# Kernel tuning notes

Measured on AMD Instinct MI355X. Metric: run time of the kernel, lower is better.

Reference implementation:

```python
import jax, jax.numpy as jnp
import numpy as np

N = 20000      # nodes
E = 320000     # edges (before self-loops)
F_IN = 512     # input feature size
HID = 128      # encoder hidden
OUT = 128      # encoder output / GAT in_channels
H = 4          # gat heads
C = 64         # gat out_channels per head


def setup_inputs() -> dict:
    key = jax.random.key(0)
    ks = jax.random.split(key, 10)
    s = 0.05
    return {
        "x": jax.random.normal(ks[0], (N, F_IN), jnp.float32),
        "edge_index": jax.random.randint(ks[1], (2, E), 0, N, dtype=jnp.int64),
        "W1": jax.random.normal(ks[2], (F_IN, HID), jnp.float32) * s,
        "b1": jax.random.normal(ks[3], (HID,), jnp.float32) * s,
        "W2": jax.random.normal(ks[4], (HID, OUT), jnp.float32) * s,
        "b2": jax.random.normal(ks[5], (OUT,), jnp.float32) * s,
        "Wg": jax.random.normal(ks[6], (OUT, H * C), jnp.float32) * s,
        "att_src": jax.random.normal(ks[7], (H, C), jnp.float32) * s,
        "att_dst": jax.random.normal(ks[8], (H, C), jnp.float32) * s,
        "bias_g": jax.random.normal(ks[9], (H * C,), jnp.float32) * s,
    }


def reference(x, edge_index, W1, b1, W2, b2, Wg, att_src, att_dst, bias_g):
    # MLP encoder: Linear -> ReLU -> Linear
    h = jnp.maximum(x @ W1 + b1, 0.0) @ W2 + b2            # [N, OUT]

    # GATConv (concat=True, eval mode -> no dropout)
    xg = (h @ Wg).reshape(N, H, C)                          # per-head projections

    # add self-loops (PyG GATConv default)
    loops = jnp.arange(N, dtype=edge_index.dtype)
    src = jnp.concatenate([edge_index[0], loops])           # [E+N] source j
    dst = jnp.concatenate([edge_index[1], loops])           # [E+N] dest   i

    a_src = jnp.einsum('nhc,hc->nh', xg, att_src)           # [N, H]
    a_dst = jnp.einsum('nhc,hc->nh', xg, att_dst)           # [N, H]

    e = jax.nn.leaky_relu(a_src[src] + a_dst[dst], 0.2)     # [E+N, H]

    # segment softmax over incoming edges of each destination node
    m = jax.ops.segment_max(e, dst, num_segments=N)         # [N, H]
    ex = jnp.exp(e - m[dst])
    denom = jax.ops.segment_sum(ex, dst, num_segments=N)
    alpha = ex / (denom[dst] + 1e-16)                       # [E+N, H]

    # weighted scatter-add aggregation
    out = jax.ops.segment_sum(alpha[:, :, None] * xg[src], dst, num_segments=N)  # [N, H, C]
    return out.reshape(N, H * C) + bias_g
```

## Files before the change

kernel.cpp:

```cpp
#include <hip/hip_runtime.h>
#include <math.h>

#define NNODES 20000
#define NEDGES 320000
#define FIN    512
#define HIDD   128
#define OUTD   128
#define NH     4
#define NC     64
#define HC     256

typedef short bf16x8 __attribute__((ext_vector_type(8)));
typedef float f32x4  __attribute__((ext_vector_type(4)));

__device__ __forceinline__ unsigned short f2bf(float f) {
    unsigned int u = __float_as_uint(f);
    unsigned int r = 0x7fffu + ((u >> 16) & 1u);
    return (unsigned short)((u + r) >> 16);
}
__device__ __forceinline__ float b2f(short t) {
    return __uint_as_float(((unsigned)(unsigned short)t) << 16);
}
__device__ __forceinline__ float4 f4max(float4 a, float4 b) {
    return make_float4(fmaxf(a.x,b.x), fmaxf(a.y,b.y), fmaxf(a.z,b.z), fmaxf(a.w,b.w));
}
__device__ __forceinline__ float4 f4add(float4 a, float4 b) {
    return make_float4(a.x+b.x, a.y+b.y, a.z+b.z, a.w+b.w);
}
__device__ __forceinline__ float4 f4sub(float4 a, float4 b) {
    return make_float4(a.x-b.x, a.y-b.y, a.z-b.z, a.w-b.w);
}
__device__ __forceinline__ float4 f4mul(float4 a, float4 b) {
    return make_float4(a.x*b.x, a.y*b.y, a.z*b.z, a.w*b.w);
}
__device__ __forceinline__ float4 f4exp(float4 a) {
    return make_float4(__expf(a.x), __expf(a.y), __expf(a.z), __expf(a.w));
}
__device__ __forceinline__ float4 shflx4(float4 v, int m) {
    return make_float4(__shfl_xor(v.x,m), __shfl_xor(v.y,m), __shfl_xor(v.z,m), __shfl_xor(v.w,m));
}

__global__ __launch_bounds__(256)
void prep_kernel(const float* __restrict__ W1, unsigned short* __restrict__ W1t,
                 const float* __restrict__ W2, const float* __restrict__ b2,
                 const float* __restrict__ Wg, unsigned short* __restrict__ W2gt,
                 float* __restrict__ b2g, int* __restrict__ deg, int n) {
    const int T1 = FIN * HIDD;
    const int T2 = HC * HIDD;
    int idx = blockIdx.x * 256 + threadIdx.x;
    if (idx < T1) {
        int nn = idx / FIN, k = idx % FIN;
        W1t[idx] = f2bf(W1[(size_t)k * HIDD + nn]);
    } else if (idx < T1 + T2) {
        int local = idx - T1;
        int nn = local >> 7;
        int k  = local & 127;
        float s = 0.f;
        #pragma unroll 8
        for (int t = 0; t < HIDD; ++t)
            s += W2[(size_t)k * OUTD + t] * Wg[(size_t)t * HC + nn];
        W2gt[(size_t)nn * HIDD + k] = f2bf(s);
        if (k == 0) {
            float t2 = 0.f;
            #pragma unroll 8
            for (int t = 0; t < OUTD; ++t) t2 += b2[t] * Wg[(size_t)t * HC + nn];
            b2g[nn] = t2;
        }
    } else if (idx < T1 + T2 + n) {
        deg[idx - T1 - T2] = 1;
    }
}

__global__ __launch_bounds__(256)
void gemm1_count_kernel(const float* __restrict__ A,
                        const unsigned short* __restrict__ Bt,
                        const float* __restrict__ bias,
                        unsigned short* __restrict__ C,
                        const int* __restrict__ dst, int* __restrict__ deg,
                        int M, int E, int gemmBlocks) {
    __shared__ unsigned short As[32 * 64];
    __shared__ unsigned short Bs[128 * 64];

    if ((int)blockIdx.x >= gemmBlocks) {
        int i = ((int)blockIdx.x - gemmBlocks) * 256 + threadIdx.x;
        if (i < E) atomicAdd(&deg[dst[i]], 1);
        return;
    }

    const int tid  = threadIdx.x;
    const int lane = tid & 63;
    const int w    = tid >> 6;
    const int wr   = w >> 1;
    const int wc   = w & 1;
    const int m0   = blockIdx.x * 32;

    char* pA = (char*)As;
    char* pB = (char*)Bs;

    f32x4 acc[4];
    #pragma unroll
    for (int n = 0; n < 4; ++n) acc[n] = (f32x4){0.f, 0.f, 0.f, 0.f};

    for (int k0 = 0; k0 < FIN; k0 += 64) {
        {
            const int row = tid >> 3;
            const int sg  = tid & 7;
            const bool ok = (m0 + row) < M;
            const float4* Ap = (const float4*)(A + (size_t)(m0 + row) * FIN + k0 + sg * 8);
            float4 f0 = make_float4(0,0,0,0), f1 = f0;
            if (ok) { f0 = Ap[0]; f1 = Ap[1]; }
            unsigned short u[8];
            u[0]=f2bf(f0.x); u[1]=f2bf(f0.y); u[2]=f2bf(f0.z); u[3]=f2bf(f0.w);
            u[4]=f2bf(f1.x); u[5]=f2bf(f1.y); u[6]=f2bf(f1.z); u[7]=f2bf(f1.w);
            *(bf16x8*)(pA + (((row * 128 + sg * 16)) ^ ((row & 7) << 4))) = *(bf16x8*)&u[0];
        }
        #pragma unroll
        for (int i = 0; i < 4; ++i) {
            int s   = tid + i * 256;
            int col = s >> 3;
            int sg  = s & 7;
            bf16x8 v = *(const bf16x8*)(Bt + (size_t)col * FIN + k0 + sg * 8);
            *(bf16x8*)(pB + (((col * 128 + sg * 16)) ^ ((col & 7) << 4))) = v;
        }
        __syncthreads();

        #pragma unroll
        for (int ks = 0; ks < 2; ++ks) {
            const int kb = ks * 64 + ((lane >> 4) << 4);
            int row = wr * 16 + (lane & 15);
            bf16x8 a = *(const bf16x8*)(pA + ((row * 128 + kb) ^ ((row & 7) << 4)));
            bf16x8 b[4];
            #pragma unroll
            for (int n = 0; n < 4; ++n) {
                int col = wc * 64 + n * 16 + (lane & 15);
                b[n] = *(const bf16x8*)(pB + ((col * 128 + kb) ^ ((col & 7) << 4)));
            }
            #pragma unroll
            for (int n = 0; n < 4; ++n)
                acc[n] = __builtin_amdgcn_mfma_f32_16x16x32_bf16(a, b[n], acc[n], 0, 0, 0);
        }
        __syncthreads();
    }

    #pragma unroll
    for (int n = 0; n < 4; ++n) {
        const int col = wc * 64 + n * 16 + (lane & 15);
        const float bv = bias[col];
        #pragma unroll
        for (int r = 0; r < 4; ++r) {
            const int row = m0 + wr * 16 + ((lane >> 4) << 2) + r;
            if (row >= M) continue;
            float v = fmaxf(acc[n][r] + bv, 0.f);
            C[(size_t)row * HIDD + col] = f2bf(v);
        }
    }
}

__global__ __launch_bounds__(256)
void gemm2_dots_kernel(const unsigned short* __restrict__ Ab,
                       const unsigned short* __restrict__ Bt,
                       const float* __restrict__ b2g,
                       const float* __restrict__ att_src,
                       const float* __restrict__ att_dst,
                       unsigned short* __restrict__ xgb,
                       float* __restrict__ a_src, float* __restrict__ a_dst,
                       int M) {
    __shared__ unsigned short As[64 * 64];
    __shared__ unsigned short Bs[128 * 64];

    const int tid  = threadIdx.x;
    const int lane = tid & 63;
    const int w    = tid >> 6;
    const int wr   = w >> 1;
    const int wc   = w & 1;
    const int m0   = blockIdx.x * 64;
    const int n0   = blockIdx.y * 128;

    char* pA = (char*)As;
    char* pB = (char*)Bs;

    f32x4 acc[2][4];
    #pragma unroll
    for (int m = 0; m < 2; ++m)
        #pragma unroll
        for (int n = 0; n < 4; ++n) acc[m][n] = (f32x4){0.f, 0.f, 0.f, 0.f};

    for (int k0 = 0; k0 < HIDD; k0 += 64) {
        #pragma unroll
        for (int i = 0; i < 2; ++i) {
            int s   = tid + i * 256;
            int row = s >> 3;
            int sg  = s & 7;
            bf16x8 v = {};
            if ((m0 + row) < M)
                v = *(const bf16x8*)(Ab + (size_t)(m0 + row) * HIDD + k0 + sg * 8);
            *(bf16x8*)(pA + (((row * 128 + sg * 16)) ^ ((row & 7) << 4))) = v;
        }
        #pragma unroll
        for (int i = 0; i < 4; ++i) {
            int s   = tid + i * 256;
            int col = s >> 3;
            int sg  = s & 7;
            bf16x8 v = *(const bf16x8*)(Bt + (size_t)(n0 + col) * HIDD + k0 + sg * 8);
            *(bf16x8*)(pB + (((col * 128 + sg * 16)) ^ ((col & 7) << 4))) = v;
        }
        __syncthreads();

        #pragma unroll
        for (int ks = 0; ks < 2; ++ks) {
            const int kb = ks * 64 + ((lane >> 4) << 4);
            bf16x8 a[2], b[4];
            #pragma unroll
            for (int m = 0; m < 2; ++m) {
                int row = wr * 32 + m * 16 + (lane & 15);
                a[m] = *(const bf16x8*)(pA + ((row * 128 + kb) ^ ((row & 7) << 4)));
            }
            #pragma unroll
            for (int n = 0; n < 4; ++n) {
                int col = wc * 64 + n * 16 + (lane & 15);
                b[n] = *(const bf16x8*)(pB + ((col * 128 + kb) ^ ((col & 7) << 4)));
            }
            #pragma unroll
            for (int m = 0; m < 2; ++m)
                #pragma unroll
                for (int n = 0; n < 4; ++n)
                    acc[m][n] = __builtin_amdgcn_mfma_f32_16x16x32_bf16(
                        a[m], b[n], acc[m][n], 0, 0, 0);
        }
        __syncthreads();
    }

    const int head = blockIdx.y * 2 + wc;
    const int cIn  = lane & 15;
    float ds_p[2][4], dd_p[2][4];
    #pragma unroll
    for (int m = 0; m < 2; ++m)
        #pragma unroll
        for (int r = 0; r < 4; ++r) { ds_p[m][r] = 0.f; dd_p[m][r] = 0.f; }

    #pragma unroll
    for (int n = 0; n < 4; ++n) {
        const int ch  = n * 16 + cIn;
        const int col = n0 + wc * 64 + n * 16 + cIn;
        const float bv   = b2g[col];
        const float as_c = att_src[head * NC + ch];
        const float ad_c = att_dst[head * NC + ch];
        #pragma unroll
        for (int m = 0; m < 2; ++m) {
            #pragma unroll
            for (int r = 0; r < 4; ++r) {
                const int row = m0 + wr * 32 + m * 16 + ((lane >> 4) << 2) + r;
                float v = acc[m][n][r] + bv;
                if (row < M) xgb[(size_t)row * HC + col] = f2bf(v);
                ds_p[m][r] += v * as_c;
                dd_p[m][r] += v * ad_c;
            }
        }
    }
    #pragma unroll
    for (int m = 0; m < 2; ++m) {
        #pragma unroll
        for (int r = 0; r < 4; ++r) {
            float s = ds_p[m][r], d = dd_p[m][r];
            s += __shfl_xor(s, 1); s += __shfl_xor(s, 2);
            s += __shfl_xor(s, 4); s += __shfl_xor(s, 8);
            d += __shfl_xor(d, 1); d += __shfl_xor(d, 2);
            d += __shfl_xor(d, 4); d += __shfl_xor(d, 8);
            if (cIn == 0) {
                const int row = m0 + wr * 32 + m * 16 + ((lane >> 4) << 2) + r;
                if (row < M) {
                    a_src[row * NH + head] = s;
                    a_dst[row * NH + head] = d;
                }
            }
        }
    }
}

__global__ __launch_bounds__(1024)
void scan_offsets_kernel(const int* __restrict__ deg, int* __restrict__ offs,
                         int* __restrict__ cursor, int n) {
    __shared__ int wsum[16], wbase[16];
    const int tid = threadIdx.x, lane = tid & 63, w = tid >> 6;
    const int i0 = tid * 20;
    int loc[20];
    int s = 0;
    #pragma unroll
    for (int k = 0; k < 20; ++k) {
        int i = i0 + k;
        int v = (i < n) ? deg[i] : 0;
        loc[k] = s;
        s += v;
    }
    int incl = s;
    #pragma unroll
    for (int d = 1; d < 64; d <<= 1) {
        int t = __shfl_up(incl, d);
        if (lane >= d) incl += t;
    }
    if (lane == 63) wsum[w] = incl;
    __syncthreads();
    if (w == 0) {
        int v = (lane < 16) ? wsum[lane] : 0;
        int sc = v;
        #pragma unroll
        for (int d = 1; d < 16; d <<= 1) {
            int t = __shfl_up(sc, d);
            if (lane >= d) sc += t;
        }
        if (lane < 16) wbase[lane] = sc - v;
    }
    __syncthreads();
    const int excl = wbase[w] + incl - s;
    #pragma unroll
    for (int k = 0; k < 20; ++k) {
        int i = i0 + k;
        if (i < n) { int o = excl + loc[k]; offs[i] = o; cursor[i] = o; }
    }
    if (tid == 1023) offs[n] = excl + s;
}

__global__ void scatter_kernel(const int* __restrict__ src, const int* __restrict__ dst,
                               int* __restrict__ cursor, int* __restrict__ csr_src,
                               int e, int n) {
    int i = blockIdx.x * 256 + threadIdx.x;
    if (i < e) {
        int s = src[i], d = dst[i];
        csr_src[atomicAdd(&cursor[d], 1)] = s;
    } else if (i < e + n) {
        int node = i - e;
        csr_src[atomicAdd(&cursor[node], 1)] = node;
    }
}

__global__ __launch_bounds__(256)
void gat_aggregate4_kernel(const unsigned short* __restrict__ xgb,
                           const float4* __restrict__ asrc4,
                           const float4* __restrict__ adst4,
                           const int* __restrict__ offs, const int* __restrict__ csr_src,
                           const float* __restrict__ bias, float* __restrict__ out, int n) {
    __shared__ float4 exbuf[4][64];
    __shared__ int    sbuf[4][64];
    const int wv   = threadIdx.x >> 6;
    const int lane = threadIdx.x & 63;
    const int node = blockIdx.x * 4 + wv;
    if (node >= n) return;
    const int beg = offs[node], end = offs[node + 1];
    const int deg = end - beg;
    const float4 adstv = adst4[node];

    float4 m   = make_float4(-INFINITY, -INFINITY, -INFINITY, -INFINITY);
    float4 den = make_float4(0.f, 0.f, 0.f, 0.f);
    for (int c0 = 0; c0 < deg; c0 += 64) {
        int idx = beg + c0 + lane;
        bool ok = idx < end;
        int s = ok ? csr_src[idx] : 0;
        float4 e = make_float4(-INFINITY, -INFINITY, -INFINITY, -INFINITY);
        if (ok) {
            float4 a = asrc4[s];
            e = f4add(a, adstv);
            e.x = e.x > 0.f ? e.x : 0.2f * e.x;
            e.y = e.y > 0.f ? e.y : 0.2f * e.y;
            e.z = e.z > 0.f ? e.z : 0.2f * e.z;
            e.w = e.w > 0.f ? e.w : 0.2f * e.w;
        }
        float4 cm = e;
        #pragma unroll
        for (int dd = 32; dd >= 1; dd >>= 1) cm = f4max(cm, shflx4(cm, dd));
        float4 nm = f4max(m, cm);
        float4 ex = f4exp(f4sub(e, nm));
        exbuf[wv][lane] = ex;
        sbuf[wv][lane]  = s;
        float4 cs = ex;
        #pragma unroll
        for (int dd = 32; dd >= 1; dd >>= 1) cs = f4add(cs, shflx4(cs, dd));
        den = f4add(f4mul(den, f4exp(f4sub(m, nm))), cs);
        m = nm;
    }

    const int hi = lane >> 5;
    const int ll = lane & 31;
    const int h  = ll >> 3;
    const float denh = (h == 0) ? den.x : (h == 1) ? den.y : (h == 2) ? den.z : den.w;
    const float inv = 1.f / (denh + 1e-16f);

    float4 acc0 = make_float4(0.f, 0.f, 0.f, 0.f);
    float4 acc1 = make_float4(0.f, 0.f, 0.f, 0.f);
    const float* exf = (const float*)&exbuf[wv][0];

    auto do_edge = [&](int jj) {
        int s = sbuf[wv][jj];
        float wgt = exf[jj * 4 + h];
        bf16x8 v = *(const bf16x8*)(xgb + (size_t)s * HC + ll * 8);
        acc0.x += wgt * b2f(v[0]); acc0.y += wgt * b2f(v[1]);
        acc0.z += wgt * b2f(v[2]); acc0.w += wgt * b2f(v[3]);
        acc1.x += wgt * b2f(v[4]); acc1.y += wgt * b2f(v[5]);
        acc1.z += wgt * b2f(v[6]); acc1.w += wgt * b2f(v[7]);
    };

    auto run_chunk = [&](int cn) {
        int j = 0;
        for (; j + 16 <= cn; j += 16) {
            int ss[8]; float ww[8]; bf16x8 vv[8];
            #pragma unroll
            for (int t = 0; t < 8; ++t) {
                int jj = j + 2 * t + hi;
                ss[t] = sbuf[wv][jj];
                ww[t] = exf[jj * 4 + h];
            }
            #pragma unroll
            for (int t = 0; t < 8; ++t)
                vv[t] = *(const bf16x8*)(xgb + (size_t)ss[t] * HC + ll * 8);
            #pragma unroll
            for (int t = 0; t < 8; ++t) {
                acc0.x += ww[t]*b2f(vv[t][0]); acc0.y += ww[t]*b2f(vv[t][1]);
                acc0.z += ww[t]*b2f(vv[t][2]); acc0.w += ww[t]*b2f(vv[t][3]);
                acc1.x += ww[t]*b2f(vv[t][4]); acc1.y += ww[t]*b2f(vv[t][5]);
                acc1.z += ww[t]*b2f(vv[t][6]); acc1.w += ww[t]*b2f(vv[t][7]);
            }
        }
        for (; j + 8 <= cn; j += 8) {
            do_edge(j + hi);     do_edge(j + 2 + hi);
            do_edge(j + 4 + hi); do_edge(j + 6 + hi);
        }
        for (; j + 4 <= cn; j += 4) {
            do_edge(j + hi);
            do_edge(j + 2 + hi);
        }
        for (; j < cn; j += 2) {
            int jj = j + hi;
            if (jj < cn) do_edge(jj);
        }
    };

    if (deg <= 64) {
        run_chunk(deg);
    } else {
        for (int c0 = 0; c0 < deg; c0 += 64) {
            int idx = beg + c0 + lane;
            if (idx < end) {
                int s = csr_src[idx];
                float4 e = f4add(asrc4[s], adstv);
                e.x = e.x > 0.f ? e.x : 0.2f * e.x;
                e.y = e.y > 0.f ? e.y : 0.2f * e.y;
                e.z = e.z > 0.f ? e.z : 0.2f * e.z;
                e.w = e.w > 0.f ? e.w : 0.2f * e.w;
                exbuf[wv][lane] = f4exp(f4sub(e, m));
                sbuf[wv][lane]  = s;
            }
            int cn = deg - c0; if (cn > 64) cn = 64;
            run_chunk(cn);
        }
    }

    acc0.x += __shfl_xor(acc0.x, 32); acc0.y += __shfl_xor(acc0.y, 32);
    acc0.z += __shfl_xor(acc0.z, 32); acc0.w += __shfl_xor(acc0.w, 32);
    acc1.x += __shfl_xor(acc1.x, 32); acc1.y += __shfl_xor(acc1.y, 32);
    acc1.z += __shfl_xor(acc1.z, 32); acc1.w += __shfl_xor(acc1.w, 32);

    const float4* b4 = (const float4*)bias;
    float4* op = (float4*)(out + (size_t)node * HC);
    if (hi == 0) {
        float4 bv = b4[ll * 2];
        op[ll * 2] = make_float4(acc0.x * inv + bv.x, acc0.y * inv + bv.y,
                                 acc0.z * inv + bv.z, acc0.w * inv + bv.w);
    } else {
        float4 bv = b4[ll * 2 + 1];
        op[ll * 2 + 1] = make_float4(acc1.x * inv + bv.x, acc1.y * inv + bv.y,
                                     acc1.z * inv + bv.z, acc1.w * inv + bv.w);
    }
}

extern "C" void kernel_launch(void* const* d_in, const int* in_sizes, int n_in,
                              void* d_out, int out_size, void* d_ws, size_t ws_size,
                              hipStream_t stream) {
    const float* x       = (const float*)d_in[0];
    const int*   ei      = (const int*)d_in[1];
    const float* W1      = (const float*)d_in[2];
    const float* b1      = (const float*)d_in[3];
    const float* W2      = (const float*)d_in[4];
    const float* b2      = (const float*)d_in[5];
    const float* Wg      = (const float*)d_in[6];
    const float* att_src = (const float*)d_in[7];
    const float* att_dst = (const float*)d_in[8];
    const float* bias_g  = (const float*)d_in[9];

    const int Nn = in_sizes[0] / FIN;
    const int E  = in_sizes[1] / 2;
    const int* e_src = ei;
    const int* e_dst = ei + E;

    char* w = (char*)d_ws;
    auto alloc = [&](size_t bytes) { char* p = w; w += (bytes + 255) & ~(size_t)255; return p; };
    unsigned short* W1t  = (unsigned short*)alloc((size_t)OUTD * FIN * 2);
    unsigned short* W2gt = (unsigned short*)alloc((size_t)HC * HIDD * 2);
    float* b2g  = (float*)alloc(HC * 4);
    unsigned short* h1  = (unsigned short*)alloc((size_t)Nn * HIDD * 2);
    unsigned short* xgb = (unsigned short*)alloc((size_t)Nn * HC * 2);
    float* asrc = (float*)alloc((size_t)Nn * NH * 4);
    float* adst = (float*)alloc((size_t)Nn * NH * 4);
    int* deg    = (int*)alloc((size_t)Nn * 4);
    int* offs   = (int*)alloc((size_t)(Nn + 1) * 4);
    int* cursor = (int*)alloc((size_t)Nn * 4);
    int* csr    = (int*)alloc((size_t)(E + Nn) * 4);

    dim3 blk(256);

    {
        int total = FIN * HIDD + HC * HIDD + Nn;
        prep_kernel<<<dim3((total + 255) / 256), blk, 0, stream>>>(
            W1, W1t, W2, b2, Wg, W2gt, b2g, deg, Nn);
    }

    {
        int gb = (Nn + 31) / 32;
        int cb = (E + 255) / 256;
        gemm1_count_kernel<<<dim3(gb + cb), blk, 0, stream>>>(
            x, W1t, b1, h1, e_dst, deg, Nn, E, gb);
    }

    gemm2_dots_kernel<<<dim3((Nn + 63) / 64, 2), blk, 0, stream>>>(
        h1, W2gt, b2g, att_src, att_dst, xgb, asrc, adst, Nn);

    scan_offsets_kernel<<<dim3(1), dim3(1024), 0, stream>>>(deg, offs, cursor, Nn);
    scatter_kernel<<<dim3((E + Nn + 255) / 256), blk, 0, stream>>>(
        e_src, e_dst, cursor, csr, E, Nn);

    gat_aggregate4_kernel<<<dim3((Nn + 3) / 4), blk, 0, stream>>>(
        xgb, (const float4*)asrc, (const float4*)adst, offs, csr, bias_g,
        (float*)d_out, Nn);
}
```

Baseline: 127.0 us.

## Fold degree scan into gemm2 launch, pre-place self-loops, tile W1 transpose

The single-block prefix scan of node degrees now runs as an extra block inside the gemm2 launch instead of as its own kernel. That block writes each node's self-loop entry directly into the CSR and starts the cursor one past it, so the scatter kernel only handles real edges. The W1 transpose in the prep kernel now goes through a 32x32 shared-memory tile so both reads and writes are coalesced. This removes one launch and some atomics. The cost is that the scan becomes a serial loop over 256-element chunks in one block, which could become the slowest block of the gemm2 grid.

```diff
diff --git a/kernel.cpp b/kernel.cpp
--- a/kernel.cpp
+++ b/kernel.cpp
@@ -40,19 +40,35 @@
     return make_float4(__shfl_xor(v.x,m), __shfl_xor(v.y,m), __shfl_xor(v.z,m), __shfl_xor(v.w,m));
 }
 
+#define PREP_TB1 64
+#define PREP_TB2 192
 __global__ __launch_bounds__(256)
 void prep_kernel(const float* __restrict__ W1, unsigned short* __restrict__ W1t,
                  const float* __restrict__ W2, const float* __restrict__ b2,
                  const float* __restrict__ Wg, unsigned short* __restrict__ W2gt,
                  float* __restrict__ b2g, int* __restrict__ deg, int n) {
-    const int T1 = FIN * HIDD;
-    const int T2 = HC * HIDD;
-    int idx = blockIdx.x * 256 + threadIdx.x;
-    if (idx < T1) {
-        int nn = idx / FIN, k = idx % FIN;
-        W1t[idx] = f2bf(W1[(size_t)k * HIDD + nn]);
-    } else if (idx < T1 + T2) {
-        int local = idx - T1;
+    const int bid = blockIdx.x;
+    const int tid = threadIdx.x;
+    if (bid < PREP_TB1) {
+        __shared__ float tile[32][33];
+        const int tk = bid >> 2;
+        const int tn = bid & 3;
+        const int k0 = tk * 32, n0 = tn * 32;
+        const int nin = tid & 31;
+        const int r8  = tid >> 5;
+        #pragma unroll
+        for (int s = 0; s < 4; ++s) {
+            int k = s * 8 + r8;
+            tile[k][nin] = W1[(size_t)(k0 + k) * HIDD + n0 + nin];
+        }
+        __syncthreads();
+        #pragma unroll
+        for (int s = 0; s < 4; ++s) {
+            int nn = s * 8 + r8;
+            W1t[(size_t)(n0 + nn) * FIN + k0 + nin] = f2bf(tile[nin][nn]);
+        }
+    } else if (bid < PREP_TB2) {
+        int local = (bid - PREP_TB1) * 256 + tid;
         int nn = local >> 7;
         int k  = local & 127;
         float s = 0.f;
@@ -66,8 +82,9 @@
             for (int t = 0; t < OUTD; ++t) t2 += b2[t] * Wg[(size_t)t * HC + nn];
             b2g[nn] = t2;
         }
-    } else if (idx < T1 + T2 + n) {
-        deg[idx - T1 - T2] = 1;
+    } else {
+        int i = (bid - PREP_TB2) * 256 + tid;
+        if (i < n) deg[i] = 1;
     }
 }
 
@@ -157,18 +174,58 @@
 }
 
 __global__ __launch_bounds__(256)
-void gemm2_dots_kernel(const unsigned short* __restrict__ Ab,
-                       const unsigned short* __restrict__ Bt,
-                       const float* __restrict__ b2g,
-                       const float* __restrict__ att_src,
-                       const float* __restrict__ att_dst,
-                       unsigned short* __restrict__ xgb,
-                       float* __restrict__ a_src, float* __restrict__ a_dst,
-                       int M) {
+void gemm2_dots_scan_kernel(const unsigned short* __restrict__ Ab,
+                            const unsigned short* __restrict__ Bt,
+                            const float* __restrict__ b2g,
+                            const float* __restrict__ att_src,
+                            const float* __restrict__ att_dst,
+                            unsigned short* __restrict__ xgb,
+                            float* __restrict__ a_src, float* __restrict__ a_dst,
+                            const int* __restrict__ deg, int* __restrict__ offs,
+                            int* __restrict__ cursor, int* __restrict__ csr,
+                            int M, int gemmX) {
+    const int tid  = threadIdx.x;
+
+    if ((int)blockIdx.x == gemmX) {
+        if (blockIdx.y != 0) return;
+        __shared__ int wsum_s[4];
+        __shared__ int carry_s;
+        const int lane = tid & 63;
+        const int wv   = tid >> 6;
+        if (tid == 0) carry_s = 0;
+        __syncthreads();
+        for (int c0 = 0; c0 < M; c0 += 256) {
+            int i = c0 + tid;
+            int v = (i < M) ? deg[i] : 0;
+            int s = v;
+            #pragma unroll
+            for (int d = 1; d < 64; d <<= 1) {
+                int t = __shfl_up(s, d);
+                if (lane >= d) s += t;
+            }
+            if (lane == 63) wsum_s[wv] = s;
+            __syncthreads();
+            int base = carry_s;
+            int wpre = 0;
+            #pragma unroll
+            for (int t = 0; t < 4; ++t) if (t < wv) wpre += wsum_s[t];
+            int excl = base + wpre + s - v;
+            if (i < M) {
+                offs[i]   = excl;
+                cursor[i] = excl + 1;
+                csr[excl] = i;
+            }
+            __syncthreads();
+            if (tid == 255) carry_s = base + wpre + s;
+            __syncthreads();
+        }
+        if (tid == 0) offs[M] = carry_s;
+        return;
+    }
+
     __shared__ unsigned short As[64 * 64];
     __shared__ unsigned short Bs[128 * 64];
 
-    const int tid  = threadIdx.x;
     const int lane = tid & 63;
     const int w    = tid >> 6;
     const int wr   = w >> 1;
@@ -277,59 +334,13 @@
     }
 }
 
-__global__ __launch_bounds__(1024)
-void scan_offsets_kernel(const int* __restrict__ deg, int* __restrict__ offs,
-                         int* __restrict__ cursor, int n) {
-    __shared__ int wsum[16], wbase[16];
-    const int tid = threadIdx.x, lane = tid & 63, w = tid >> 6;
-    const int i0 = tid * 20;
-    int loc[20];
-    int s = 0;
-    #pragma unroll
-    for (int k = 0; k < 20; ++k) {
-        int i = i0 + k;
-        int v = (i < n) ? deg[i] : 0;
-        loc[k] = s;
-        s += v;
-    }
-    int incl = s;
-    #pragma unroll
-    for (int d = 1; d < 64; d <<= 1) {
-        int t = __shfl_up(incl, d);
-        if (lane >= d) incl += t;
-    }
-    if (lane == 63) wsum[w] = incl;
-    __syncthreads();
-    if (w == 0) {
-        int v = (lane < 16) ? wsum[lane] : 0;
-        int sc = v;
-        #pragma unroll
-        for (int d = 1; d < 16; d <<= 1) {
-            int t = __shfl_up(sc, d);
-            if (lane >= d) sc += t;
-        }
-        if (lane < 16) wbase[lane] = sc - v;
-    }
-    __syncthreads();
-    const int excl = wbase[w] + incl - s;
-    #pragma unroll
-    for (int k = 0; k < 20; ++k) {
-        int i = i0 + k;
-        if (i < n) { int o = excl + loc[k]; offs[i] = o; cursor[i] = o; }
-    }
-    if (tid == 1023) offs[n] = excl + s;
-}
-
 __global__ void scatter_kernel(const int* __restrict__ src, const int* __restrict__ dst,
                                int* __restrict__ cursor, int* __restrict__ csr_src,
-                               int e, int n) {
+                               int e) {
     int i = blockIdx.x * 256 + threadIdx.x;
     if (i < e) {
         int s = src[i], d = dst[i];
         csr_src[atomicAdd(&cursor[d], 1)] = s;
-    } else if (i < e + n) {
-        int node = i - e;
-        csr_src[atomicAdd(&cursor[node], 1)] = node;
     }
 }
 
@@ -507,8 +518,8 @@
     dim3 blk(256);
 
     {
-        int total = FIN * HIDD + HC * HIDD + Nn;
-        prep_kernel<<<dim3((total + 255) / 256), blk, 0, stream>>>(
+        int nb = PREP_TB2 + (Nn + 255) / 256;
+        prep_kernel<<<dim3(nb), blk, 0, stream>>>(
             W1, W1t, W2, b2, Wg, W2gt, b2g, deg, Nn);
     }
 
@@ -519,12 +530,15 @@
             x, W1t, b1, h1, e_dst, deg, Nn, E, gb);
     }
 
-    gemm2_dots_kernel<<<dim3((Nn + 63) / 64, 2), blk, 0, stream>>>(
-        h1, W2gt, b2g, att_src, att_dst, xgb, asrc, adst, Nn);
-
-    scan_offsets_kernel<<<dim3(1), dim3(1024), 0, stream>>>(deg, offs, cursor, Nn);
-    scatter_kernel<<<dim3((E + Nn + 255) / 256), blk, 0, stream>>>(
-        e_src, e_dst, cursor, csr, E, Nn);
+    {
+        int gx = (Nn + 63) / 64;
+        gemm2_dots_scan_kernel<<<dim3(gx + 1, 2), blk, 0, stream>>>(
+            h1, W2gt, b2g, att_src, att_dst, xgb, asrc, adst,
+            deg, offs, cursor, csr, Nn, gx);
+    }
+
+    scatter_kernel<<<dim3((E + 255) / 256), blk, 0, stream>>>(
+        e_src, e_dst, cursor, csr, E);
 
     gat_aggregate4_kernel<<<dim3((Nn + 3) / 4), blk, 0, stream>>>(
         xgb, (const float4*)asrc, (const float4*)adst, offs, csr, bias_g,
```

Measured after the change: 147.6 us. +16.2%, slower.
